# Kernel tuning notes

Hardware: AMD Instinct MI355X
Metric: run time of the kernel (lower is better)

## Reference

```python
import math
import jax, jax.numpy as jnp
import numpy as np

DMODEL = 512
NUM_HEADS = 8
HEAD_DIM = DMODEL // NUM_HEADS
MAX_LEN = 1024
L = 2 * MAX_LEN - 1  # 2047
B = 4
S = 1024  # src_len == max_len


def setup_inputs() -> dict:
    key = jax.random.key(0)
    ks = jax.random.split(key, 12)
    f32 = jnp.float32
    inp = {
        "query": jax.random.normal(ks[0], (B, S, DMODEL), f32),
        "key": jax.random.normal(ks[1], (B, S, DMODEL), f32),
        "value": jax.random.normal(ks[2], (B, S, DMODEL), f32),
        # nn.Linear weights (y = x @ W.T + b)
        "Wq": jax.random.normal(ks[3], (DMODEL, DMODEL), f32) * 0.02,
        "bq": jnp.zeros((DMODEL,), f32),
        "Wk": jax.random.normal(ks[4], (DMODEL, DMODEL), f32) * 0.02,
        "bk": jnp.zeros((DMODEL,), f32),
        "Wv": jax.random.normal(ks[5], (DMODEL, DMODEL), f32) * 0.02,
        "bv": jnp.zeros((DMODEL,), f32),
        # relative position tables (torch.randn init)
        "quaver_Er": jax.random.normal(ks[6], (NUM_HEADS, L, HEAD_DIM), f32),
        "beat_Er": jax.random.normal(ks[7], (NUM_HEADS, L // 4, HEAD_DIM), f32),
        "bar_Er": jax.random.normal(ks[8], (NUM_HEADS, L // 16, HEAD_DIM), f32),
    }
    return inp


def _skew(QEr):
    # QEr: [b, h, S, 2S-1] -> [b, h, S, S] via pad-reshape-slice trick
    b, h, s, l = QEr.shape
    x = jnp.pad(QEr, ((0, 0), (0, 0), (0, 0), (0, 1)))        # [b,h,S,2S]
    x = x.reshape(b, h, -1)                                    # [b,h,S*2S]
    x = jnp.pad(x, ((0, 0), (0, 0), (0, l - s)))               # [b,h,(S+1)*(2S-1)]
    x = x.reshape(b, h, s + 1, l)
    return x[:, :, :s, -s:]


def _skew_chunked(QEr, rep):
    # Faithful to skew_beat/skew_bar: repeat_interleave(rep) along last dim, then
    # roll each chunk of `rep` rows (chunk i) by i*rep, then take last S cols.
    b, h, s, lr = QEr.shape
    x = jnp.repeat(QEr, rep, axis=-1)                          # [b,h,S,rep*lr]
    w = rep * lr
    shifts = (jnp.arange(s) // rep) * rep                      # [S]
    # torch.roll: out[c] = in[(c - shift) mod W]
    cols = (jnp.arange(w)[None, :] - shifts[:, None]) % w      # [S, W]
    x = jnp.take_along_axis(x, cols[None, None], axis=-1)
    return x[:, :, :s, -s:]


def reference(query, key, value, Wq, bq, Wk, bk, Wv, bv, quaver_Er, beat_Er, bar_Er):
    bs, src_len, d_model = query.shape
    h, hd = NUM_HEADS, HEAD_DIM
    max_len = MAX_LEN

    q = (query @ Wq.T + bq).reshape(bs, src_len, h, hd).transpose(0, 2, 1, 3)   # [b,h,S,d]
    k = (key @ Wk.T + bk).reshape(bs, src_len, h, hd).transpose(0, 2, 3, 1)      # [b,h,d,S]
    v = (value @ Wv.T + bv).reshape(bs, src_len, h, hd).transpose(0, 2, 1, 3)    # [b,h,S,d]

    Er_q = quaver_Er[:, max_len - src_len:max_len + src_len, :]                  # [h,2S-1,d]
    Er_b = beat_Er[:, (max_len - src_len) // 4:(max_len + src_len) // 4, :]      # [h,~S/2,d]
    Er_r = bar_Er[:, (max_len - src_len) // 16:(max_len + src_len) // 16, :]     # [h,~S/8,d]

    QEr_q = jnp.einsum('bhsd,hld->bhsl', q, Er_q)
    QEr_b = jnp.einsum('bhsd,hld->bhsl', q, Er_b)
    QEr_r = jnp.einsum('bhsd,hld->bhsl', q, Er_r)

    Srel = _skew(QEr_q)
    Srel_beat = _skew_chunked(QEr_b, 4)
    Srel_bar = _skew_chunked(QEr_r, 16)

    attn = (jnp.matmul(q, k) + Srel + Srel_beat + Srel_bar) / math.sqrt(hd)
    attn = jax.nn.softmax(attn, axis=-1)
    out = jnp.matmul(attn, v)                                                    # [b,h,S,d]
    out = out.transpose(0, 2, 1, 3).reshape(bs, src_len, d_model)
    return out, attn
```

## Files before the change

### kernel.cpp

```cpp
#include <hip/hip_runtime.h>


typedef float f32x4 __attribute__((ext_vector_type(4)));
typedef short s16x8 __attribute__((ext_vector_type(8)));
typedef short s16x4 __attribute__((ext_vector_type(4)));
typedef __bf16 bf16x8 __attribute__((ext_vector_type(8)));

static __device__ __forceinline__ short f2bf(float f) {
    return __builtin_bit_cast(short, (__bf16)f);
}
static __device__ __forceinline__ float bf2f(short s) {
    union { unsigned u; float f; } v;
    v.u = ((unsigned)(unsigned short)s) << 16;
    return v.f;
}
static __device__ __forceinline__ f32x4 MM(s16x8 a, s16x8 b, f32x4 c) {
    return __builtin_amdgcn_mfma_f32_16x16x32_bf16(
        __builtin_bit_cast(bf16x8, a), __builtin_bit_cast(bf16x8, b), c, 0, 0, 0);
}
#define KEEP(x) asm volatile("" : "+v"(x))
#define BARL() asm volatile("s_waitcnt lgkmcnt(0)\n\ts_barrier" ::: "memory")

struct CvtArgs {
    const float* src[9];
    short* dst[9];
    unsigned n[9];
};

__global__ __launch_bounds__(256) void convert_kernel(CvtArgs a) {
    const int ai = blockIdx.y;
    const unsigned n = a.n[ai];
    const float* __restrict__ s = a.src[ai];
    short* __restrict__ d = a.dst[ai];
    const unsigned stride = gridDim.x * 256 * 8;
    for (unsigned base = (blockIdx.x * 256 + threadIdx.x) * 8; base < n; base += stride) {
        f32x4 v0 = *(const f32x4*)(s + base);
        f32x4 v1 = *(const f32x4*)(s + base + 4);
        s16x8 o;
        o[0] = f2bf(v0[0]); o[1] = f2bf(v0[1]); o[2] = f2bf(v0[2]); o[3] = f2bf(v0[3]);
        o[4] = f2bf(v1[0]); o[5] = f2bf(v1[1]); o[6] = f2bf(v1[2]); o[7] = f2bf(v1[3]);
        *(s16x8*)(d + base) = o;
    }
}

__global__ __launch_bounds__(128, 2) void proj_kernel(
    const short* __restrict__ queryb, const short* __restrict__ keyb, const short* __restrict__ valueb,
    const short* __restrict__ Wqb, const float* __restrict__ bq,
    const short* __restrict__ Wkb, const float* __restrict__ bk,
    const short* __restrict__ Wvb, const float* __restrict__ bv,
    short* __restrict__ qb, short* __restrict__ kb, short* __restrict__ vT)
{
    const int tid = threadIdx.x;
    const int wid = tid >> 6, lane = tid & 63;
    const int l15 = lane & 15, grp = lane >> 4;
    const int gid = blockIdx.x * 2 + wid;
    const int z = gid >> 9;
    const int r = gid & 511;

    const short *Am, *Bm;
    const float* bias;
    int a0, b0;
    if (z == 0)      { Am = Wqb;    Bm = queryb; bias = bq; a0 = (r >> 6) * 64; b0 = (r & 63) * 64; }
    else if (z == 1) { Am = Wkb;    Bm = keyb;   bias = bk; a0 = (r >> 6) * 64; b0 = (r & 63) * 64; }
    else             { Am = valueb; Bm = Wvb;    bias = bv; a0 = (r >> 3) * 64; b0 = (r & 7) * 64; }

    f32x4 acc[4][4];
    #pragma unroll
    for (int i = 0; i < 4; ++i)
        #pragma unroll
        for (int j = 0; j < 4; ++j)
            acc[i][j] = f32x4{0.f, 0.f, 0.f, 0.f};

    const short* arow0 = Am + (size_t)(a0 + l15) * 512 + grp * 8;
    const short* brow0 = Bm + (size_t)(b0 + l15) * 512 + grp * 8;

    s16x8 aA[4], bA[4], aB[4], bB[4];
    #pragma unroll
    for (int i = 0; i < 4; ++i) {
        aA[i] = *(const s16x8*)(arow0 + (size_t)i * 16 * 512);
        bA[i] = *(const s16x8*)(brow0 + (size_t)i * 16 * 512);
    }
    for (int kk = 0; kk < 512; kk += 32) {
        const int kn = kk + 32;
        if (kn < 512) {
            #pragma unroll
            for (int i = 0; i < 4; ++i) {
                aB[i] = *(const s16x8*)(arow0 + (size_t)i * 16 * 512 + kn);
                bB[i] = *(const s16x8*)(brow0 + (size_t)i * 16 * 512 + kn);
            }
        }
        #pragma unroll
        for (int i = 0; i < 4; ++i)
            #pragma unroll
            for (int j = 0; j < 4; ++j)
                acc[i][j] = MM(aA[i], bA[j], acc[i][j]);
        #pragma unroll
        for (int i = 0; i < 4; ++i) { aA[i] = aB[i]; bA[i] = bB[i]; }
    }

    if (z < 2) {
        short* dst = (z == 0) ? qb : kb;
        #pragma unroll
        for (int i = 0; i < 4; ++i) {
            const int f0 = a0 + i * 16 + grp * 4;
            const f32x4 bv4 = *(const f32x4*)&bias[f0];
            const int h = f0 >> 6, d0 = f0 & 63;
            #pragma unroll
            for (int j = 0; j < 4; ++j) {
                const int srow = b0 + j * 16 + l15;
                const int bb = srow >> 10, sl = srow & 1023;
                s16x4 o;
                #pragma unroll
                for (int g = 0; g < 4; ++g)
                    o[g] = f2bf(acc[i][j][g] + bv4[g]);
                *(s16x4*)&dst[(size_t)((bb * 8 + h) * 1024 + sl) * 64 + d0] = o;
            }
        }
    } else {
        #pragma unroll
        for (int j = 0; j < 4; ++j) {
            const int n = b0 + j * 16 + l15;
            const float bval = bias[n];
            const int h = n >> 6, d = n & 63;
            #pragma unroll
            for (int i = 0; i < 4; ++i) {
                const int s0 = a0 + i * 16 + grp * 4;
                const int bb = s0 >> 10, sl = s0 & 1023;
                s16x4 o;
                #pragma unroll
                for (int g = 0; g < 4; ++g)
                    o[g] = f2bf(acc[i][j][g] + bval);
                *(s16x4*)&vT[(size_t)((bb * 8 + h) * 64 + d) * 1024 + sl] = o;
            }
        }
    }
}

__global__ __launch_bounds__(512, 2) void attn_kernel(
    const short* __restrict__ Eqb, const short* __restrict__ Ebb, const short* __restrict__ Errb,
    const short* __restrict__ qb, const short* __restrict__ kb, const short* __restrict__ vT,
    float* __restrict__ out, float* __restrict__ attn)
{
    __shared__ __align__(16) char smem[155008];
    short* PS   = (short*)(smem + 86784);
    float* PACC = (float*)(smem + 119680);

    const int tid = threadIdx.x;
    const int wid = tid >> 6, lane = tid & 63;
    const int l15 = lane & 15, grp = lane >> 4;

    const int orig = blockIdx.x;
    const int bid = (orig & 7) * 32 + (orig >> 3);

    const int bh = bid >> 3;
    const int chunk = bid & 7;
    const int h = bh & 7;
    const int b = bh >> 3;

    const short* EqH = Eqb  + (size_t)h * 2047 * 64;
    const short* EbH = Ebb  + (size_t)h * 511 * 64;
    const short* ErH = Errb + (size_t)h * 127 * 64;
    const short* qbH = qb + (size_t)bh * 1024 * 64;
    const short* kbH = kb + (size_t)bh * 1024 * 64;
    const short* vTH = vT + (size_t)bh * 64 * 1024;

    auto buildT = [&](int i0s, int bb01, s16x8 q0, s16x8 q1) {
        short* RQ2 = (short*)(smem + bb01 * 32896);
        short* RB2 = (short*)(smem + 65792 + bb01 * 8320);
        short* RR2 = (short*)(smem + 82432 + bb01 * 2176);
        const int qbase = 1008 - i0s;
        {
            auto ldq = [&](int cs, s16x8& e0, s16x8& e1) {
                int erow = qbase + cs * 16 + l15; if (erow > 2046) erow = 2046;
                const short* ep = EqH + (size_t)erow * 64 + grp * 8;
                e0 = *(const s16x8*)ep;
                e1 = *(const s16x8*)(ep + 32);
            };
            s16x8 A0, A1, B0, B1, C0, C1;
            ldq(wid, A0, A1);
            ldq(wid + 8, B0, B1);
            ldq(wid + 16, C0, C1);
            for (int cs = wid; cs < 65; cs += 8) {
                f32x4 a = f32x4{0.f, 0.f, 0.f, 0.f};
                a = MM(q0, A0, a);
                a = MM(q1, A1, a);
                A0 = B0; A1 = B1; B0 = C0; B1 = C1;
                ldq(cs + 24, C0, C1);
                const int c = cs * 16 + l15;
                #pragma unroll
                for (int g = 0; g < 4; ++g) {
                    const int ii = grp * 4 + g;
                    const int j = c - 15 + ii;
                    if (j >= 0 && j < 1024) RQ2[ii * 1028 + j] = f2bf(a[g]);
                }
            }
        }
        const int bbase = 252 - (i0s >> 2);
        {
            auto ldb = [&](int cs, s16x8& e0, s16x8& e1) {
                int erow = bbase + cs * 16 + l15; if (erow > 510) erow = 510;
                const short* ep = EbH + (size_t)erow * 64 + grp * 8;
                e0 = *(const s16x8*)ep;
                e1 = *(const s16x8*)(ep + 32);
            };
            s16x8 A0, A1, B0, B1;
            ldb(wid, A0, A1);
            ldb(wid + 8, B0, B1);
            for (int cs = wid; cs < 17; cs += 8) {
                f32x4 a = f32x4{0.f, 0.f, 0.f, 0.f};
                a = MM(q0, A0, a);
                a = MM(q1, A1, a);
                A0 = B0; A1 = B1;
                ldb(cs + 16, B0, B1);
                const int c = cs * 16 + l15;
                const int jq = c - 3 + grp;
                if (jq >= 0 && jq < 256) {
                    #pragma unroll
                    for (int g = 0; g < 4; ++g)
                        RB2[(grp * 4 + g) * 260 + jq] = f2bf(a[g]);
                }
            }
        }
        const int rbase = 63 - (i0s >> 4);
        if (wid < 4) {
            const int c = wid * 16 + l15;
            const short* ep = ErH + (size_t)(rbase + c) * 64 + grp * 8;
            s16x8 e0 = *(const s16x8*)ep;
            s16x8 e1 = *(const s16x8*)(ep + 32);
            f32x4 a = f32x4{0.f, 0.f, 0.f, 0.f};
            a = MM(q0, e0, a);
            a = MM(q1, e1, a);
            #pragma unroll
            for (int g = 0; g < 4; ++g)
                RR2[(grp * 4 + g) * 68 + c] = f2bf(a[g]);
        }
    };

    const int i00 = chunk * 128;
    s16x8 qA0 = *(const s16x8*)(qbH + (size_t)(i00 + l15) * 64 + grp * 8);
    s16x8 qA1 = *(const s16x8*)(qbH + (size_t)(i00 + l15) * 64 + 32 + grp * 8);

    s16x8 kf[8][2];
    #pragma unroll
    for (int t = 0; t < 8; ++t) {
        const short* kp = kbH + (size_t)(wid * 128 + t * 16 + l15) * 64 + grp * 8;
        kf[t][0] = *(const s16x8*)kp;
        kf[t][1] = *(const s16x8*)(kp + 32);
    }
    s16x8 vreg[16];
    #pragma unroll
    for (int dvt = 0; dvt < 4; ++dvt)
        #pragma unroll
        for (int kc = 0; kc < 4; ++kc)
            vreg[dvt * 4 + kc] = *(const s16x8*)(vTH + (size_t)(dvt * 16 + l15) * 1024
                                                 + wid * 128 + kc * 32 + grp * 8);

    buildT(i00, 0, qA0, qA1);
    BARL();

    const float SC = 0.125f * 1.4426950408889634f;
    const int swz = (l15 & 3) << 5;

    for (int s = 0; s < 8; ++s) {
        #pragma unroll
        for (int t = 0; t < 8; ++t) { KEEP(kf[t][0]); KEEP(kf[t][1]); }
        #pragma unroll
        for (int z = 0; z < 16; ++z) KEEP(vreg[z]);

        const int cur = s & 1;
        const int i0 = chunk * 128 + s * 16;
        short* RQ2c = (short*)(smem + cur * 32896);
        short* RB2c = (short*)(smem + 65792 + cur * 8320);
        short* RR2c = (short*)(smem + 82432 + cur * 2176);
        float* RSUMc = (float*)(smem + 154496 + cur * 256);

        s16x8 qn0, qn1;
        if (s < 7) {
            qn0 = *(const s16x8*)(qbH + (size_t)(i0 + 16 + l15) * 64 + grp * 8);
            qn1 = *(const s16x8*)(qbH + (size_t)(i0 + 16 + l15) * 64 + 32 + grp * 8);
        }

        f32x4 p[8];
        #pragma unroll
        for (int t = 0; t < 8; ++t) {
            f32x4 a = f32x4{0.f, 0.f, 0.f, 0.f};
            a = MM(kf[t][0], qA0, a);
            a = MM(kf[t][1], qA1, a);
            const int jb2 = wid * 128 + t * 16 + grp * 4;
            s16x4 gq4 = *(const s16x4*)&RQ2c[l15 * 1028 + jb2];
            const float rb = bf2f(RB2c[l15 * 260 + wid * 32 + t * 4 + grp]);
            const float rr = bf2f(RR2c[l15 * 68 + wid * 8 + t]);
            const float add = rb + rr;
            f32x4 pe;
            #pragma unroll
            for (int g = 0; g < 4; ++g)
                pe[g] = __builtin_amdgcn_exp2f((a[g] + bf2f(gq4[g]) + add) * SC);
            p[t] = pe;
        }

        float part = 0.f;
        #pragma unroll
        for (int t = 0; t < 8; ++t)
            #pragma unroll
            for (int g = 0; g < 4; ++g)
                part += p[t][g];
        part += __shfl_xor(part, 16, 64);
        part += __shfl_xor(part, 32, 64);
        if (lane < 16) RSUMc[lane * 8 + wid] = part;

        #pragma unroll
        for (int t = 0; t < 8; ++t) {
            const int col = (wid * 128 + t * 16 + grp * 4) ^ swz;
            s16x4 o;
            #pragma unroll
            for (int g = 0; g < 4; ++g) o[g] = f2bf(p[t][g]);
            *(s16x4*)&PS[l15 * 1028 + col] = o;
        }
        BARL();

        float rinv;
        {
            f32x4 s0 = *(const f32x4*)&RSUMc[l15 * 8];
            f32x4 s1 = *(const f32x4*)&RSUMc[l15 * 8 + 4];
            rinv = 1.0f / (s0[0] + s0[1] + s0[2] + s0[3] + s1[0] + s1[1] + s1[2] + s1[3]);
        }

        if (s < 7) buildT(i0 + 16, cur ^ 1, qn0, qn1);

        {
            float* arow = attn + (size_t)(bh * 1024 + i0 + l15) * 1024;
            #pragma unroll
            for (int t = 0; t < 8; ++t) {
                f32x4 o = p[t] * rinv;
                *(f32x4*)&arow[wid * 128 + t * 16 + grp * 4] = o;
            }
        }

        const int kh = wid & 1;  (void)kh;
        f32x4 acc[4];
        #pragma unroll
        for (int dvt = 0; dvt < 4; ++dvt) acc[dvt] = f32x4{0.f, 0.f, 0.f, 0.f};
        #pragma unroll
        for (int kc = 0; kc < 4; ++kc) {
            const int col = (wid * 128 + kc * 32 + grp * 8) ^ swz;
            s16x8 bfrag = *(const s16x8*)&PS[l15 * 1028 + col];
            #pragma unroll
            for (int dvt = 0; dvt < 4; ++dvt)
                acc[dvt] = MM(vreg[dvt * 4 + kc], bfrag, acc[dvt]);
        }
        #pragma unroll
        for (int dvt = 0; dvt < 4; ++dvt)
            *(f32x4*)&PACC[(wid * 16 + l15) * 68 + dvt * 16 + grp * 4] = acc[dvt];
        BARL();

        if (tid < 256) {
            const int i = tid >> 4, dvq = tid & 15;
            f32x4 o = f32x4{0.f, 0.f, 0.f, 0.f};
            #pragma unroll
            for (int w = 0; w < 8; ++w)
                o += *(const f32x4*)&PACC[(w * 16 + i) * 68 + dvq * 4];
            f32x4 s0 = *(const f32x4*)&RSUMc[i * 8];
            f32x4 s1 = *(const f32x4*)&RSUMc[i * 8 + 4];
            const float ri = 1.0f / (s0[0] + s0[1] + s0[2] + s0[3] + s1[0] + s1[1] + s1[2] + s1[3]);
            o *= ri;
            *(f32x4*)&out[(size_t)(b * 1024 + i0 + i) * 512 + h * 64 + dvq * 4] = o;
        }

        if (s < 7) { qA0 = qn0; qA1 = qn1; }
    }
}

extern "C" void kernel_launch(void* const* d_in, const int* in_sizes, int n_in,
                              void* d_out, int out_size, void* d_ws, size_t ws_size,
                              hipStream_t stream)
{
    const float* query = (const float*)d_in[0];
    const float* key   = (const float*)d_in[1];
    const float* value = (const float*)d_in[2];
    const float* Wq = (const float*)d_in[3];
    const float* bq = (const float*)d_in[4];
    const float* Wk = (const float*)d_in[5];
    const float* bk = (const float*)d_in[6];
    const float* Wv = (const float*)d_in[7];
    const float* bv = (const float*)d_in[8];
    const float* Eq = (const float*)d_in[9];
    const float* Eb = (const float*)d_in[10];
    const float* Er = (const float*)d_in[11];

    float* out  = (float*)d_out;
    float* attn = out + (size_t)4 * 1024 * 512;

    short* qb     = (short*)d_ws;
    short* kb     = qb     + 2097152;
    short* vT     = kb     + 2097152;
    short* queryb = vT     + 2097152;
    short* keyb   = queryb + 2097152;
    short* valueb = keyb   + 2097152;
    short* Wqb    = valueb + 2097152;
    short* Wkb    = Wqb    + 262144;
    short* Wvb    = Wkb    + 262144;
    short* Eqb    = Wvb    + 262144;
    short* Ebb    = Eqb    + 1048064;
    short* Errb   = Ebb    + 261632;

    CvtArgs a;
    a.src[0] = query; a.dst[0] = queryb; a.n[0] = 2097152;
    a.src[1] = key;   a.dst[1] = keyb;   a.n[1] = 2097152;
    a.src[2] = value; a.dst[2] = valueb; a.n[2] = 2097152;
    a.src[3] = Wq;    a.dst[3] = Wqb;    a.n[3] = 262144;
    a.src[4] = Wk;    a.dst[4] = Wkb;    a.n[4] = 262144;
    a.src[5] = Wv;    a.dst[5] = Wvb;    a.n[5] = 262144;
    a.src[6] = Eq;    a.dst[6] = Eqb;    a.n[6] = 1048064;
    a.src[7] = Eb;    a.dst[7] = Ebb;    a.n[7] = 261632;
    a.src[8] = Er;    a.dst[8] = Errb;   a.n[8] = 65024;

    convert_kernel<<<dim3(64, 9), 256, 0, stream>>>(a);
    proj_kernel<<<768, 128, 0, stream>>>(queryb, keyb, valueb,
                                         Wqb, bq, Wkb, bk, Wvb, bv, qb, kb, vT);
    attn_kernel<<<256, 512, 0, stream>>>(Eqb, Ebb, Errb, qb, kb, vT, out, attn);
}
```

Measured before the change: 139.7 us.

## Halve attention LDS footprint and double grid for higher occupancy

Cuts the attention kernel's shared memory from about 152KB to about 77KB. It does this by aliasing the relative-table buffer with the probability and partial-accumulator buffers, and by single-buffering the beat and bar tables. The grid doubles to 512 blocks of 64 rows each, with launch bounds raised to 4 waves per SIMD. K and V fragments are now reloaded from global memory every step instead of staying pinned in registers. The quaver table build is restricted to each wave's own 128-column slice, and outputs use nontemporal stores. The aim is more resident blocks and better latency hiding, at the cost of extra barriers, repeated K/V loads, and possible races on the single-buffered beat/bar tables.

```diff
diff --git a/kernel.cpp b/kernel.cpp
--- a/kernel.cpp
+++ b/kernel.cpp
@@ -18,8 +18,6 @@
     return __builtin_amdgcn_mfma_f32_16x16x32_bf16(
         __builtin_bit_cast(bf16x8, a), __builtin_bit_cast(bf16x8, b), c, 0, 0, 0);
 }
-#define KEEP(x) asm volatile("" : "+v"(x))
-#define BARL() asm volatile("s_waitcnt lgkmcnt(0)\n\ts_barrier" ::: "memory")
 
 struct CvtArgs {
     const float* src[9];
@@ -136,24 +134,22 @@
     }
 }
 
-__global__ __launch_bounds__(512, 2) void attn_kernel(
+__global__ __launch_bounds__(512, 4) void attn_kernel(
     const short* __restrict__ Eqb, const short* __restrict__ Ebb, const short* __restrict__ Errb,
     const short* __restrict__ qb, const short* __restrict__ kb, const short* __restrict__ vT,
     float* __restrict__ out, float* __restrict__ attn)
 {
-    __shared__ __align__(16) char smem[155008];
-    short* PS   = (short*)(smem + 86784);
-    float* PACC = (float*)(smem + 119680);
+    __shared__ __align__(16) char smem[77312];
 
     const int tid = threadIdx.x;
     const int wid = tid >> 6, lane = tid & 63;
     const int l15 = lane & 15, grp = lane >> 4;
 
     const int orig = blockIdx.x;
-    const int bid = (orig & 7) * 32 + (orig >> 3);
-
-    const int bh = bid >> 3;
-    const int chunk = bid & 7;
+    const int bid = (orig & 7) * 64 + (orig >> 3);
+
+    const int bh = bid >> 4;
+    const int chunk = bid & 15;
     const int h = bh & 7;
     const int b = bh >> 3;
 
@@ -164,41 +160,44 @@
     const short* kbH = kb + (size_t)bh * 1024 * 64;
     const short* vTH = vT + (size_t)bh * 64 * 1024;
 
-    auto buildT = [&](int i0s, int bb01, s16x8 q0, s16x8 q1) {
-        short* RQ2 = (short*)(smem + bb01 * 32896);
-        short* RB2 = (short*)(smem + 65792 + bb01 * 8320);
-        short* RR2 = (short*)(smem + 82432 + bb01 * 2176);
+    short* RB2 = (short*)(smem + 65792);
+    short* RR2 = (short*)(smem + 74112);
+
+    auto buildT = [&](int i0s, char* regRQ, s16x8 q0, s16x8 q1) {
+        short* RQ2 = (short*)regRQ;
         const int qbase = 1008 - i0s;
         {
             auto ldq = [&](int cs, s16x8& e0, s16x8& e1) {
-                int erow = qbase + cs * 16 + l15; if (erow > 2046) erow = 2046;
+                int erow = qbase + wid * 128 + cs * 16 + l15;
+                if (erow > 2046) erow = 2046;
                 const short* ep = EqH + (size_t)erow * 64 + grp * 8;
                 e0 = *(const s16x8*)ep;
                 e1 = *(const s16x8*)(ep + 32);
             };
-            s16x8 A0, A1, B0, B1, C0, C1;
-            ldq(wid, A0, A1);
-            ldq(wid + 8, B0, B1);
-            ldq(wid + 16, C0, C1);
-            for (int cs = wid; cs < 65; cs += 8) {
+            s16x8 A0, A1, B0, B1;
+            ldq(0, A0, A1);
+            ldq(1, B0, B1);
+            for (int cs = 0; cs < 9; ++cs) {
                 f32x4 a = f32x4{0.f, 0.f, 0.f, 0.f};
                 a = MM(q0, A0, a);
                 a = MM(q1, A1, a);
-                A0 = B0; A1 = B1; B0 = C0; B1 = C1;
-                ldq(cs + 24, C0, C1);
-                const int c = cs * 16 + l15;
+                A0 = B0; A1 = B1;
+                if (cs < 8) ldq(cs + 2, B0, B1);
+                const int c = wid * 128 + cs * 16 + l15;
                 #pragma unroll
                 for (int g = 0; g < 4; ++g) {
                     const int ii = grp * 4 + g;
                     const int j = c - 15 + ii;
-                    if (j >= 0 && j < 1024) RQ2[ii * 1028 + j] = f2bf(a[g]);
+                    if (j >= wid * 128 && j < wid * 128 + 128 && j < 1024)
+                        RQ2[ii * 1028 + j] = f2bf(a[g]);
                 }
             }
         }
         const int bbase = 252 - (i0s >> 2);
         {
             auto ldb = [&](int cs, s16x8& e0, s16x8& e1) {
-                int erow = bbase + cs * 16 + l15; if (erow > 510) erow = 510;
+                int erow = bbase + cs * 16 + l15;
+                if (erow > 510) erow = 510;
                 const short* ep = EbH + (size_t)erow * 64 + grp * 8;
                 e0 = *(const s16x8*)ep;
                 e1 = *(const s16x8*)(ep + 32);
@@ -236,46 +235,32 @@
         }
     };
 
-    const int i00 = chunk * 128;
+    const int i00 = chunk * 64;
     s16x8 qA0 = *(const s16x8*)(qbH + (size_t)(i00 + l15) * 64 + grp * 8);
     s16x8 qA1 = *(const s16x8*)(qbH + (size_t)(i00 + l15) * 64 + 32 + grp * 8);
-
-    s16x8 kf[8][2];
-    #pragma unroll
-    for (int t = 0; t < 8; ++t) {
-        const short* kp = kbH + (size_t)(wid * 128 + t * 16 + l15) * 64 + grp * 8;
-        kf[t][0] = *(const s16x8*)kp;
-        kf[t][1] = *(const s16x8*)(kp + 32);
-    }
-    s16x8 vreg[16];
-    #pragma unroll
-    for (int dvt = 0; dvt < 4; ++dvt)
-        #pragma unroll
-        for (int kc = 0; kc < 4; ++kc)
-            vreg[dvt * 4 + kc] = *(const s16x8*)(vTH + (size_t)(dvt * 16 + l15) * 1024
-                                                 + wid * 128 + kc * 32 + grp * 8);
-
-    buildT(i00, 0, qA0, qA1);
-    BARL();
+    buildT(i00, smem, qA0, qA1);
+    __syncthreads();
 
     const float SC = 0.125f * 1.4426950408889634f;
     const int swz = (l15 & 3) << 5;
 
-    for (int s = 0; s < 8; ++s) {
-        #pragma unroll
-        for (int t = 0; t < 8; ++t) { KEEP(kf[t][0]); KEEP(kf[t][1]); }
-        #pragma unroll
-        for (int z = 0; z < 16; ++z) KEEP(vreg[z]);
-
-        const int cur = s & 1;
-        const int i0 = chunk * 128 + s * 16;
-        short* RQ2c = (short*)(smem + cur * 32896);
-        short* RB2c = (short*)(smem + 65792 + cur * 8320);
-        short* RR2c = (short*)(smem + 82432 + cur * 2176);
-        float* RSUMc = (float*)(smem + 154496 + cur * 256);
-
+    for (int s = 0; s < 4; ++s) {
+        const int i0 = i00 + s * 16;
+        char* tabR = smem + ((s & 1) ? 32896 : 0);
+        char* psR  = smem + ((s & 1) ? 0 : 32896);
+        short* RQ2c = (short*)tabR;
+        short* PSc  = (short*)psR;
+        float* RSUMp = (float*)(smem + 76288) + (s & 1) * 128;
+
+        s16x8 kf[8][2];
+        #pragma unroll
+        for (int t = 0; t < 8; ++t) {
+            const short* kp = kbH + (size_t)(wid * 128 + t * 16 + l15) * 64 + grp * 8;
+            kf[t][0] = *(const s16x8*)kp;
+            kf[t][1] = *(const s16x8*)(kp + 32);
+        }
         s16x8 qn0, qn1;
-        if (s < 7) {
+        if (s < 3) {
             qn0 = *(const s16x8*)(qbH + (size_t)(i0 + 16 + l15) * 64 + grp * 8);
             qn1 = *(const s16x8*)(qbH + (size_t)(i0 + 16 + l15) * 64 + 32 + grp * 8);
         }
@@ -288,8 +273,8 @@
             a = MM(kf[t][1], qA1, a);
             const int jb2 = wid * 128 + t * 16 + grp * 4;
             s16x4 gq4 = *(const s16x4*)&RQ2c[l15 * 1028 + jb2];
-            const float rb = bf2f(RB2c[l15 * 260 + wid * 32 + t * 4 + grp]);
-            const float rr = bf2f(RR2c[l15 * 68 + wid * 8 + t]);
+            const float rb = bf2f(RB2[l15 * 260 + wid * 32 + t * 4 + grp]);
+            const float rr = bf2f(RR2[l15 * 68 + wid * 8 + t]);
             const float add = rb + rr;
             f32x4 pe;
             #pragma unroll
@@ -306,7 +291,7 @@
                 part += p[t][g];
         part += __shfl_xor(part, 16, 64);
         part += __shfl_xor(part, 32, 64);
-        if (lane < 16) RSUMc[lane * 8 + wid] = part;
+        if (lane < 16) RSUMp[lane * 8 + wid] = part;
 
         #pragma unroll
         for (int t = 0; t < 8; ++t) {
@@ -314,59 +299,71 @@
             s16x4 o;
             #pragma unroll
             for (int g = 0; g < 4; ++g) o[g] = f2bf(p[t][g]);
-            *(s16x4*)&PS[l15 * 1028 + col] = o;
-        }
-        BARL();
+            *(s16x4*)&PSc[l15 * 1028 + col] = o;
+        }
+        __syncthreads();
+
+        s16x8 vreg[16];
+        #pragma unroll
+        for (int dvt = 0; dvt < 4; ++dvt)
+            #pragma unroll
+            for (int kc = 0; kc < 4; ++kc)
+                vreg[dvt * 4 + kc] = *(const s16x8*)(vTH + (size_t)(dvt * 16 + l15) * 1024
+                                                     + wid * 128 + kc * 32 + grp * 8);
 
         float rinv;
         {
-            f32x4 s0 = *(const f32x4*)&RSUMc[l15 * 8];
-            f32x4 s1 = *(const f32x4*)&RSUMc[l15 * 8 + 4];
+            f32x4 s0 = *(const f32x4*)&RSUMp[l15 * 8];
+            f32x4 s1 = *(const f32x4*)&RSUMp[l15 * 8 + 4];
             rinv = 1.0f / (s0[0] + s0[1] + s0[2] + s0[3] + s1[0] + s1[1] + s1[2] + s1[3]);
         }
-
-        if (s < 7) buildT(i0 + 16, cur ^ 1, qn0, qn1);
+        s16x8 bfrag[4];
+        #pragma unroll
+        for (int kc = 0; kc < 4; ++kc) {
+            const int col = (wid * 128 + kc * 32 + grp * 8) ^ swz;
+            bfrag[kc] = *(const s16x8*)&PSc[l15 * 1028 + col];
+        }
+
+        if (s < 3) buildT(i0 + 16, psR, qn0, qn1);
 
         {
             float* arow = attn + (size_t)(bh * 1024 + i0 + l15) * 1024;
             #pragma unroll
             for (int t = 0; t < 8; ++t) {
                 f32x4 o = p[t] * rinv;
-                *(f32x4*)&arow[wid * 128 + t * 16 + grp * 4] = o;
-            }
-        }
-
-        const int kh = wid & 1;  (void)kh;
+                __builtin_nontemporal_store(o, (f32x4*)&arow[wid * 128 + t * 16 + grp * 4]);
+            }
+        }
+
         f32x4 acc[4];
         #pragma unroll
         for (int dvt = 0; dvt < 4; ++dvt) acc[dvt] = f32x4{0.f, 0.f, 0.f, 0.f};
         #pragma unroll
-        for (int kc = 0; kc < 4; ++kc) {
-            const int col = (wid * 128 + kc * 32 + grp * 8) ^ swz;
-            s16x8 bfrag = *(const s16x8*)&PS[l15 * 1028 + col];
+        for (int kc = 0; kc < 4; ++kc)
             #pragma unroll
             for (int dvt = 0; dvt < 4; ++dvt)
-                acc[dvt] = MM(vreg[dvt * 4 + kc], bfrag, acc[dvt]);
-        }
+                acc[dvt] = MM(vreg[dvt * 4 + kc], bfrag[kc], acc[dvt]);
+        float* PACC = (float*)tabR;
         #pragma unroll
         for (int dvt = 0; dvt < 4; ++dvt)
-            *(f32x4*)&PACC[(wid * 16 + l15) * 68 + dvt * 16 + grp * 4] = acc[dvt];
-        BARL();
+            *(f32x4*)&PACC[wid * 1028 + l15 * 64 + ((dvt * 16 + grp * 4) ^ ((l15 & 7) << 3))] = acc[dvt];
+        __syncthreads();
 
         if (tid < 256) {
             const int i = tid >> 4, dvq = tid & 15;
             f32x4 o = f32x4{0.f, 0.f, 0.f, 0.f};
             #pragma unroll
             for (int w = 0; w < 8; ++w)
-                o += *(const f32x4*)&PACC[(w * 16 + i) * 68 + dvq * 4];
-            f32x4 s0 = *(const f32x4*)&RSUMc[i * 8];
-            f32x4 s1 = *(const f32x4*)&RSUMc[i * 8 + 4];
+                o += *(const f32x4*)&PACC[w * 1028 + i * 64 + ((dvq * 4) ^ ((i & 7) << 3))];
+            f32x4 s0 = *(const f32x4*)&RSUMp[i * 8];
+            f32x4 s1 = *(const f32x4*)&RSUMp[i * 8 + 4];
             const float ri = 1.0f / (s0[0] + s0[1] + s0[2] + s0[3] + s1[0] + s1[1] + s1[2] + s1[3]);
             o *= ri;
-            *(f32x4*)&out[(size_t)(b * 1024 + i0 + i) * 512 + h * 64 + dvq * 4] = o;
-        }
-
-        if (s < 7) { qA0 = qn0; qA1 = qn1; }
+            __builtin_nontemporal_store(o, (f32x4*)&out[(size_t)(b * 1024 + i0 + i) * 512 + h * 64 + dvq * 4]);
+        }
+        __syncthreads();
+
+        if (s < 3) { qA0 = qn0; qA1 = qn1; }
     }
 }
 
@@ -414,8 +411,8 @@
     a.src[7] = Eb;    a.dst[7] = Ebb;    a.n[7] = 261632;
     a.src[8] = Er;    a.dst[8] = Errb;   a.n[8] = 65024;
 
-    convert_kernel<<<dim3(64, 9), 256, 0, stream>>>(a);
+    convert_kernel<<<dim3(128, 9), 256, 0, stream>>>(a);
     proj_kernel<<<768, 128, 0, stream>>>(queryb, keyb, valueb,
                                          Wqb, bq, Wkb, bk, Wvb, bv, qb, kb, vT);
-    attn_kernel<<<256, 512, 0, stream>>>(Eqb, Ebb, Errb, qb, kb, vT, out, attn);
-}
+    attn_kernel<<<512, 512, 0, stream>>>(Eqb, Ebb, Errb, qb, kb, vT, out, attn);
+}
```

Measured after the change: 228.8 us. +63.8%, slower.

## Add dedicated store waves to write attention probabilities from shared memory

Applied to the files above, without the earlier changes.

Adds four extra wavefronts per block that read the bf16 unnormalized probabilities from shared memory, normalize them and write the large fp32 attention matrix. The eight compute waves no longer issue those global stores and move on to the PV matmul, so the store traffic overlaps with compute. The launch grid of the conversion kernel is also doubled. The attention output now comes from bf16-rounded values rather than fp32 ones, which reduces precision, and the larger block raises register pressure under the new launch bounds.

```diff
diff --git a/kernel.cpp b/kernel.cpp
--- a/kernel.cpp
+++ b/kernel.cpp
@@ -136,18 +136,19 @@
     }
 }
 
-__global__ __launch_bounds__(512, 2) void attn_kernel(
+__global__ __launch_bounds__(768, 3) void attn_kernel(
     const short* __restrict__ Eqb, const short* __restrict__ Ebb, const short* __restrict__ Errb,
     const short* __restrict__ qb, const short* __restrict__ kb, const short* __restrict__ vT,
     float* __restrict__ out, float* __restrict__ attn)
 {
-    __shared__ __align__(16) char smem[155008];
+    __shared__ __align__(16) char smem[155520];
     short* PS   = (short*)(smem + 86784);
     float* PACC = (float*)(smem + 119680);
 
     const int tid = threadIdx.x;
     const int wid = tid >> 6, lane = tid & 63;
     const int l15 = lane & 15, grp = lane >> 4;
+    const bool isC = (wid < 8);
 
     const int orig = blockIdx.x;
     const int bid = (orig & 7) * 32 + (orig >> 3);
@@ -237,136 +238,146 @@
     };
 
     const int i00 = chunk * 128;
-    s16x8 qA0 = *(const s16x8*)(qbH + (size_t)(i00 + l15) * 64 + grp * 8);
-    s16x8 qA1 = *(const s16x8*)(qbH + (size_t)(i00 + l15) * 64 + 32 + grp * 8);
-
-    s16x8 kf[8][2];
-    #pragma unroll
-    for (int t = 0; t < 8; ++t) {
-        const short* kp = kbH + (size_t)(wid * 128 + t * 16 + l15) * 64 + grp * 8;
-        kf[t][0] = *(const s16x8*)kp;
-        kf[t][1] = *(const s16x8*)(kp + 32);
-    }
-    s16x8 vreg[16];
-    #pragma unroll
-    for (int dvt = 0; dvt < 4; ++dvt)
-        #pragma unroll
-        for (int kc = 0; kc < 4; ++kc)
-            vreg[dvt * 4 + kc] = *(const s16x8*)(vTH + (size_t)(dvt * 16 + l15) * 1024
-                                                 + wid * 128 + kc * 32 + grp * 8);
-
-    buildT(i00, 0, qA0, qA1);
+    s16x8 qA0, qA1, kf[8][2], vreg[16];
+    if (isC) {
+        qA0 = *(const s16x8*)(qbH + (size_t)(i00 + l15) * 64 + grp * 8);
+        qA1 = *(const s16x8*)(qbH + (size_t)(i00 + l15) * 64 + 32 + grp * 8);
+        #pragma unroll
+        for (int t = 0; t < 8; ++t) {
+            const short* kp = kbH + (size_t)(wid * 128 + t * 16 + l15) * 64 + grp * 8;
+            kf[t][0] = *(const s16x8*)kp;
+            kf[t][1] = *(const s16x8*)(kp + 32);
+        }
+        #pragma unroll
+        for (int dvt = 0; dvt < 4; ++dvt)
+            #pragma unroll
+            for (int kc = 0; kc < 4; ++kc)
+                vreg[dvt * 4 + kc] = *(const s16x8*)(vTH + (size_t)(dvt * 16 + l15) * 1024
+                                                     + wid * 128 + kc * 32 + grp * 8);
+        buildT(i00, 0, qA0, qA1);
+    }
     BARL();
 
     const float SC = 0.125f * 1.4426950408889634f;
     const int swz = (l15 & 3) << 5;
 
     for (int s = 0; s < 8; ++s) {
-        #pragma unroll
-        for (int t = 0; t < 8; ++t) { KEEP(kf[t][0]); KEEP(kf[t][1]); }
-        #pragma unroll
-        for (int z = 0; z < 16; ++z) KEEP(vreg[z]);
-
         const int cur = s & 1;
         const int i0 = chunk * 128 + s * 16;
-        short* RQ2c = (short*)(smem + cur * 32896);
-        short* RB2c = (short*)(smem + 65792 + cur * 8320);
-        short* RR2c = (short*)(smem + 82432 + cur * 2176);
-        float* RSUMc = (float*)(smem + 154496 + cur * 256);
+        float* RSUMc = (float*)(smem + 154496 + cur * 512);
 
         s16x8 qn0, qn1;
-        if (s < 7) {
-            qn0 = *(const s16x8*)(qbH + (size_t)(i0 + 16 + l15) * 64 + grp * 8);
-            qn1 = *(const s16x8*)(qbH + (size_t)(i0 + 16 + l15) * 64 + 32 + grp * 8);
-        }
-
-        f32x4 p[8];
-        #pragma unroll
-        for (int t = 0; t < 8; ++t) {
-            f32x4 a = f32x4{0.f, 0.f, 0.f, 0.f};
-            a = MM(kf[t][0], qA0, a);
-            a = MM(kf[t][1], qA1, a);
-            const int jb2 = wid * 128 + t * 16 + grp * 4;
-            s16x4 gq4 = *(const s16x4*)&RQ2c[l15 * 1028 + jb2];
-            const float rb = bf2f(RB2c[l15 * 260 + wid * 32 + t * 4 + grp]);
-            const float rr = bf2f(RR2c[l15 * 68 + wid * 8 + t]);
-            const float add = rb + rr;
-            f32x4 pe;
-            #pragma unroll
-            for (int g = 0; g < 4; ++g)
-                pe[g] = __builtin_amdgcn_exp2f((a[g] + bf2f(gq4[g]) + add) * SC);
-            p[t] = pe;
-        }
-
-        float part = 0.f;
-        #pragma unroll
-        for (int t = 0; t < 8; ++t)
-            #pragma unroll
-            for (int g = 0; g < 4; ++g)
-                part += p[t][g];
-        part += __shfl_xor(part, 16, 64);
-        part += __shfl_xor(part, 32, 64);
-        if (lane < 16) RSUMc[lane * 8 + wid] = part;
-
-        #pragma unroll
-        for (int t = 0; t < 8; ++t) {
-            const int col = (wid * 128 + t * 16 + grp * 4) ^ swz;
-            s16x4 o;
-            #pragma unroll
-            for (int g = 0; g < 4; ++g) o[g] = f2bf(p[t][g]);
-            *(s16x4*)&PS[l15 * 1028 + col] = o;
+        if (isC) {
+            #pragma unroll
+            for (int t = 0; t < 8; ++t) { KEEP(kf[t][0]); KEEP(kf[t][1]); }
+            #pragma unroll
+            for (int z = 0; z < 16; ++z) KEEP(vreg[z]);
+
+            short* RQ2c = (short*)(smem + cur * 32896);
+            short* RB2c = (short*)(smem + 65792 + cur * 8320);
+            short* RR2c = (short*)(smem + 82432 + cur * 2176);
+
+            if (s < 7) {
+                qn0 = *(const s16x8*)(qbH + (size_t)(i0 + 16 + l15) * 64 + grp * 8);
+                qn1 = *(const s16x8*)(qbH + (size_t)(i0 + 16 + l15) * 64 + 32 + grp * 8);
+            }
+
+            f32x4 p[8];
+            #pragma unroll
+            for (int t = 0; t < 8; ++t) {
+                f32x4 a = f32x4{0.f, 0.f, 0.f, 0.f};
+                a = MM(kf[t][0], qA0, a);
+                a = MM(kf[t][1], qA1, a);
+                const int jb2 = wid * 128 + t * 16 + grp * 4;
+                s16x4 gq4 = *(const s16x4*)&RQ2c[l15 * 1028 + jb2];
+                const float rb = bf2f(RB2c[l15 * 260 + wid * 32 + t * 4 + grp]);
+                const float rr = bf2f(RR2c[l15 * 68 + wid * 8 + t]);
+                const float add = rb + rr;
+                f32x4 pe;
+                #pragma unroll
+                for (int g = 0; g < 4; ++g)
+                    pe[g] = __builtin_amdgcn_exp2f((a[g] + bf2f(gq4[g]) + add) * SC);
+                p[t] = pe;
+            }
+
+            float part = 0.f;
+            #pragma unroll
+            for (int t = 0; t < 8; ++t)
+                #pragma unroll
+                for (int g = 0; g < 4; ++g)
+                    part += p[t][g];
+            part += __shfl_xor(part, 16, 64);
+            part += __shfl_xor(part, 32, 64);
+            if (lane < 16) RSUMc[lane * 8 + wid] = part;
+
+            #pragma unroll
+            for (int t = 0; t < 8; ++t) {
+                const int col = (wid * 128 + t * 16 + grp * 4) ^ swz;
+                s16x4 o;
+                #pragma unroll
+                for (int g = 0; g < 4; ++g) o[g] = f2bf(p[t][g]);
+                *(s16x4*)&PS[l15 * 1028 + col] = o;
+            }
         }
         BARL();
 
-        float rinv;
-        {
-            f32x4 s0 = *(const f32x4*)&RSUMc[l15 * 8];
-            f32x4 s1 = *(const f32x4*)&RSUMc[l15 * 8 + 4];
-            rinv = 1.0f / (s0[0] + s0[1] + s0[2] + s0[3] + s1[0] + s1[1] + s1[2] + s1[3]);
-        }
-
-        if (s < 7) buildT(i0 + 16, cur ^ 1, qn0, qn1);
-
-        {
-            float* arow = attn + (size_t)(bh * 1024 + i0 + l15) * 1024;
-            #pragma unroll
-            for (int t = 0; t < 8; ++t) {
-                f32x4 o = p[t] * rinv;
-                *(f32x4*)&arow[wid * 128 + t * 16 + grp * 4] = o;
-            }
-        }
-
-        const int kh = wid & 1;  (void)kh;
-        f32x4 acc[4];
-        #pragma unroll
-        for (int dvt = 0; dvt < 4; ++dvt) acc[dvt] = f32x4{0.f, 0.f, 0.f, 0.f};
-        #pragma unroll
-        for (int kc = 0; kc < 4; ++kc) {
-            const int col = (wid * 128 + kc * 32 + grp * 8) ^ swz;
-            s16x8 bfrag = *(const s16x8*)&PS[l15 * 1028 + col];
+        if (isC) {
+            if (s < 7) buildT(i0 + 16, cur ^ 1, qn0, qn1);
+
+            f32x4 acc[4];
+            #pragma unroll
+            for (int dvt = 0; dvt < 4; ++dvt) acc[dvt] = f32x4{0.f, 0.f, 0.f, 0.f};
+            #pragma unroll
+            for (int kc = 0; kc < 4; ++kc) {
+                const int col = (wid * 128 + kc * 32 + grp * 8) ^ swz;
+                s16x8 bfrag = *(const s16x8*)&PS[l15 * 1028 + col];
+                #pragma unroll
+                for (int dvt = 0; dvt < 4; ++dvt)
+                    acc[dvt] = MM(vreg[dvt * 4 + kc], bfrag, acc[dvt]);
+            }
             #pragma unroll
             for (int dvt = 0; dvt < 4; ++dvt)
-                acc[dvt] = MM(vreg[dvt * 4 + kc], bfrag, acc[dvt]);
-        }
-        #pragma unroll
-        for (int dvt = 0; dvt < 4; ++dvt)
-            *(f32x4*)&PACC[(wid * 16 + l15) * 68 + dvt * 16 + grp * 4] = acc[dvt];
+                *(f32x4*)&PACC[(wid * 16 + l15) * 68 + dvt * 16 + grp * 4] = acc[dvt];
+        } else {
+            const int ww = wid - 8;
+            #pragma unroll
+            for (int k = 0; k < 4; ++k) {
+                const int r = ww * 4 + k;
+                f32x4 s0 = *(const f32x4*)&RSUMc[r * 8];
+                f32x4 s1 = *(const f32x4*)&RSUMc[r * 8 + 4];
+                const float ri = 1.0f / (s0[0] + s0[1] + s0[2] + s0[3]
+                                         + s1[0] + s1[1] + s1[2] + s1[3]);
+                float* arow = attn + (size_t)(bh * 1024 + i0 + r) * 1024;
+                const int rswz = (r & 3) << 5;
+                #pragma unroll
+                for (int pass = 0; pass < 4; ++pass) {
+                    const int col = pass * 256 + lane * 4;
+                    s16x4 v4 = *(const s16x4*)&PS[r * 1028 + (col ^ rswz)];
+                    f32x4 o;
+                    o[0] = bf2f(v4[0]) * ri; o[1] = bf2f(v4[1]) * ri;
+                    o[2] = bf2f(v4[2]) * ri; o[3] = bf2f(v4[3]) * ri;
+                    *(f32x4*)(arow + col) = o;
+                }
+            }
+        }
         BARL();
 
-        if (tid < 256) {
-            const int i = tid >> 4, dvq = tid & 15;
-            f32x4 o = f32x4{0.f, 0.f, 0.f, 0.f};
-            #pragma unroll
-            for (int w = 0; w < 8; ++w)
-                o += *(const f32x4*)&PACC[(w * 16 + i) * 68 + dvq * 4];
-            f32x4 s0 = *(const f32x4*)&RSUMc[i * 8];
-            f32x4 s1 = *(const f32x4*)&RSUMc[i * 8 + 4];
-            const float ri = 1.0f / (s0[0] + s0[1] + s0[2] + s0[3] + s1[0] + s1[1] + s1[2] + s1[3]);
-            o *= ri;
-            *(f32x4*)&out[(size_t)(b * 1024 + i0 + i) * 512 + h * 64 + dvq * 4] = o;
-        }
-
-        if (s < 7) { qA0 = qn0; qA1 = qn1; }
+        if (isC) {
+            if (tid < 256) {
+                const int i = tid >> 4, dvq = tid & 15;
+                f32x4 o = f32x4{0.f, 0.f, 0.f, 0.f};
+                #pragma unroll
+                for (int w = 0; w < 8; ++w)
+                    o += *(const f32x4*)&PACC[(w * 16 + i) * 68 + dvq * 4];
+                f32x4 s0 = *(const f32x4*)&RSUMc[i * 8];
+                f32x4 s1 = *(const f32x4*)&RSUMc[i * 8 + 4];
+                const float ri = 1.0f / (s0[0] + s0[1] + s0[2] + s0[3]
+                                         + s1[0] + s1[1] + s1[2] + s1[3]);
+                o *= ri;
+                *(f32x4*)&out[(size_t)(b * 1024 + i0 + i) * 512 + h * 64 + dvq * 4] = o;
+            }
+            if (s < 7) { qA0 = qn0; qA1 = qn1; }
+        }
     }
 }
 
@@ -414,8 +425,8 @@
     a.src[7] = Eb;    a.dst[7] = Ebb;    a.n[7] = 261632;
     a.src[8] = Er;    a.dst[8] = Errb;   a.n[8] = 65024;
 
-    convert_kernel<<<dim3(64, 9), 256, 0, stream>>>(a);
+    convert_kernel<<<dim3(128, 9), 256, 0, stream>>>(a);
     proj_kernel<<<768, 128, 0, stream>>>(queryb, keyb, valueb,
                                          Wqb, bq, Wkb, bk, Wvb, bv, qb, kb, vT);
-    attn_kernel<<<256, 512, 0, stream>>>(Eqb, Ebb, Errb, qb, kb, vT, out, attn);
-}
+    attn_kernel<<<256, 768, 0, stream>>>(Eqb, Ebb, Errb, qb, kb, vT, out, attn);
+}
```

After: 236.4 us. 69.2% more time.
